# Kernel tuning notes

Hardware: AMD Instinct MI355X
Metric: run time of the kernel (lower is better)

The kernel has to match this reference:

```python
import jax, jax.numpy as jnp
import numpy as np

BS = 256
MAX_ARGS = 8
CTX_DIM = 128        # context_dim (local key/query dim)
NODE_DIM = 128       # node_dim (global query / embedding dim)
HIDDEN = 512
STATE_DIM = 512
TAC_DIM = 128
TOTAL_CTX = 131072   # total context nodes (~512 per batch element)
N_CLASS = 30000      # node_class_num
DEF_NUM = 20000      # len(global_context)
CTX_VAL_DIM = 256    # feature dim of context_emb.values
DIM = CTX_DIM + 1 + NODE_DIM  # 257


def setup_inputs() -> dict:
    key = jax.random.key(0)
    ks = jax.random.split(key, 12)
    ctx_ids = jnp.sort(jax.random.randint(ks[0], (TOTAL_CTX,), 0, BS)).astype(jnp.int32)
    ctx_vals = jax.random.normal(ks[1], (TOTAL_CTX, CTX_VAL_DIM), jnp.float32)
    state_emb = jax.random.normal(ks[2], (BS, STATE_DIM), jnp.float32)
    tactic_emb = jax.random.normal(ks[3], (BS, TAC_DIM), jnp.float32)
    arg_cnt = jax.random.randint(ks[4], (BS,), 0, MAX_ARGS + 1).astype(jnp.int32)
    global_context = jax.random.randint(ks[5], (DEF_NUM,), 0, N_CLASS).astype(jnp.int32)
    emb_table = jax.random.normal(ks[6], (N_CLASS, NODE_DIM), jnp.float32) * 0.05
    s1 = 1.0 / np.sqrt(CTX_VAL_DIM)
    W_key = jax.random.uniform(ks[7], (CTX_VAL_DIM, CTX_DIM), jnp.float32, -s1, s1)
    b_key = jnp.zeros((CTX_DIM,), jnp.float32)
    s2 = 1.0 / np.sqrt(STATE_DIM + TAC_DIM)
    W_st = jax.random.uniform(ks[8], (STATE_DIM + TAC_DIM, HIDDEN), jnp.float32, -s2, s2)
    b_st = jnp.zeros((HIDDEN,), jnp.float32)
    s3 = 1.0 / np.sqrt(HIDDEN)
    W_q = jax.random.uniform(ks[9], (HIDDEN, MAX_ARGS * DIM), jnp.float32, -s3, s3)
    b_q = jnp.zeros((MAX_ARGS * DIM,), jnp.float32)
    return dict(ctx_vals=ctx_vals, state_emb=state_emb, tactic_emb=tactic_emb,
                emb_table=emb_table, W_key=W_key, b_key=b_key, W_st=W_st, b_st=b_st,
                W_q=W_q, b_q=b_q, ctx_ids=ctx_ids, arg_cnt=arg_cnt,
                global_context=global_context)


def _build_indices(ctx_ids, arg_cnt, bs, max_args):
    """Host-side (numpy) reconstruction of the ragged index plumbing.
    Mirrors: sequence_mask/boolean_mask, unsorted_segment_sum, ragged.range,
    cumsum(exclusive) and the nested gathers of ArgumentLocalLogits."""
    ctx_ids = np.asarray(ctx_ids)
    arg_cnt = np.asarray(arg_cnt)
    # boolean_mask over [bs, max_args] sequence mask -> selected flat slots (row-major)
    mask = np.arange(max_args)[None, :] < arg_cnt[:, None]
    flat_sel = np.nonzero(mask.reshape(-1))[0]
    arguments_i = np.repeat(np.arange(bs), arg_cnt)          # batch id of each argument
    total_args = arguments_i.shape[0]
    ctx_lens = np.bincount(ctx_ids, minlength=bs)            # unsorted_segment_sum of ones
    ctx_starts = np.concatenate([[0], np.cumsum(ctx_lens)[:-1]])  # exclusive cumsum
    arg_ctx_lens = ctx_lens[arguments_i]
    arg_ctx_rows = np.repeat(np.arange(total_args), arg_ctx_lens)  # value_rowids of ragged.range
    pair_starts = np.concatenate([[0], np.cumsum(arg_ctx_lens)[:-1]])
    offs = np.arange(int(arg_ctx_lens.sum())) - np.repeat(pair_starts, arg_ctx_lens)
    arg_ctx_cols = ctx_starts[arguments_i][arg_ctx_rows] + offs
    return flat_sel, arg_ctx_rows, arg_ctx_cols, total_args


def reference(ctx_vals, state_emb, tactic_emb, emb_table, W_key, b_key,
              W_st, b_st, W_q, b_q, ctx_ids, arg_cnt, global_context):
    bs = state_emb.shape[0]
    flat_sel, rows, cols, total_args = _build_indices(ctx_ids, arg_cnt, bs, MAX_ARGS)
    gc = np.asarray(global_context)

    # state_tac_emb = relu(Dense(concat([state, tactic])))
    st = jax.nn.relu(jnp.concatenate([state_emb, tactic_emb], axis=1) @ W_st + b_st)
    # local_none_global: [bs, max_args, dim] -> boolean_mask -> [total_args, dim]
    lng = (st @ W_q + b_q).reshape(bs * MAX_ARGS, DIM)[flat_sel]
    local_queries = lng[:, :CTX_DIM]              # [total_args, CTX_DIM]
    none_logits = lng[:, CTX_DIM]                 # [total_args]
    global_queries = lng[:, CTX_DIM + 1:]         # [total_args, NODE_DIM]

    # local logits: gather-dot over (argument, context-node-of-its-batch) pairs
    keys = ctx_vals @ W_key + b_key               # act_key Dense: [total_ctx, CTX_DIM]
    local_flat = jnp.einsum('ij,ij->i', local_queries[rows], keys[cols])

    # global logits: unit-normalized embedding keys (normalize=True)
    gk = emb_table[gc]                            # [DEF_NUM, NODE_DIM]
    gk = gk / (1e-7 + jnp.sqrt(jnp.sum(gk * gk, axis=-1, keepdims=True)))
    global_flat = (global_queries @ gk.T).reshape(-1)  # row-major [total_args*DEF_NUM]

    indices = jnp.concatenate([
        jnp.asarray(rows, jnp.int32),
        jnp.arange(total_args, dtype=jnp.int32),
        jnp.asarray(np.repeat(np.arange(total_args), DEF_NUM), jnp.int32)])
    values = jnp.concatenate([local_flat, none_logits, global_flat])
    return indices, values
```

## Files before the change

### kernel.cpp

```cpp
#include <hip/hip_runtime.h>

#define BSZ 256
#define MAXA 8
#define CTXD 128
#define HID 512
#define STD 512
#define TACD 128
#define DEFN 20000
#define CVD 256
#define DIMQ 257
#define LNGW 2056

typedef __attribute__((ext_vector_type(8))) short bf16x8;
typedef __attribute__((ext_vector_type(4))) float f32x4;

#define O_TOT 0
#define O_NP  1
#define O_CS  16
#define O_AS  288
#define O_AB  560
#define O_SL  2608
#define O_PS  4656
#define F_GQB  8192
#define F_QB   139264
#define F_WST  141312
#define F_STB  305152
#define F_LNG  370688
#define F_WQT  897024
#define F_QK   897024
#define F_GKB  141312

__device__ __forceinline__ ushort f2bf(float f) {
    uint u = __float_as_uint(f);
    return (ushort)((u + 0x7FFFu + ((u >> 16) & 1u)) >> 16);
}

__global__ __launch_bounds__(256) void k_bounds(const int* __restrict__ ctx_ids, int n_ctx,
                                                int* __restrict__ W) {
    int i = blockIdx.x * 256 + threadIdx.x;
    if (i >= n_ctx) return;
    int cur = ctx_ids[i];
    int prev = (i == 0) ? -1 : ctx_ids[i - 1];
    for (int b = prev + 1; b <= cur; b++) W[O_CS + b] = i;
    if (i == n_ctx - 1) {
        for (int b = cur + 1; b <= BSZ; b++) W[O_CS + b] = n_ctx;
    }
}

__global__ __launch_bounds__(256) void k_scan(const int* __restrict__ arg_cnt, int* __restrict__ W) {
    __shared__ int s_start[BSZ + 1];
    __shared__ int s_len[BSZ];
    __shared__ int s_scan[BSZ];
    __shared__ int s_as[BSZ + 1];
    __shared__ int s_ab[2048];
    __shared__ int s_sl[2048];
    __shared__ int s_ps[BSZ];
    int tid = threadIdx.x;
    s_start[tid] = W[O_CS + tid];
    if (tid == 0) s_start[BSZ] = W[O_CS + BSZ];
    int c = arg_cnt[tid];
    s_scan[tid] = c;
    __syncthreads();
    s_len[tid] = s_start[tid + 1] - s_start[tid];
    for (int off = 1; off < BSZ; off <<= 1) {
        int v = s_scan[tid];
        int a = (tid >= off) ? s_scan[tid - off] : 0;
        __syncthreads();
        s_scan[tid] = v + a;
        __syncthreads();
    }
    int astart = s_scan[tid] - c;
    s_as[tid] = astart;
    if (tid == BSZ - 1) s_as[BSZ] = s_scan[tid];
    __syncthreads();
    int total = s_as[BSZ];
    for (int k = 0; k < c; k++) { s_ab[astart + k] = tid; s_sl[astart + k] = k; }
    __syncthreads();
    int base = tid * 8;
    int loc[8]; int run = 0;
    for (int j = 0; j < 8; j++) {
        int t = base + j;
        int l = (t < total) ? s_len[s_ab[t]] : 0;
        loc[j] = run; run += l;
    }
    s_ps[tid] = run;
    __syncthreads();
    for (int off = 1; off < BSZ; off <<= 1) {
        int v = s_ps[tid];
        int a = (tid >= off) ? s_ps[tid - off] : 0;
        __syncthreads();
        s_ps[tid] = v + a;
        __syncthreads();
    }
    int pbase = s_ps[tid] - run;
    int np = s_ps[BSZ - 1];
    W[O_AS + tid] = astart;
    if (tid == 0) { W[O_AS + BSZ] = total; W[O_TOT] = total; W[O_NP] = np; W[O_PS + 2048] = np; }
    for (int j = 0; j < 8; j++) {
        int t = base + j;
        W[O_PS + t] = pbase + loc[j];
        W[O_AB + t] = (t < total) ? s_ab[t] : 0;
        W[O_SL + t] = (t < total) ? s_sl[t] : 0;
    }
}

__global__ __launch_bounds__(256) void k_trans(const float* __restrict__ in, ushort* __restrict__ out,
                                               int R, int C) {
    __shared__ float t[32][33];
    int c0 = blockIdx.x * 32, r0 = blockIdx.y * 32;
    int lx = threadIdx.x & 31, ly = threadIdx.x >> 5;
    #pragma unroll
    for (int i = 0; i < 32; i += 8) {
        int r = r0 + ly + i, c = c0 + lx;
        t[ly + i][lx] = (r < R && c < C) ? in[(size_t)r * C + c] : 0.f;
    }
    __syncthreads();
    #pragma unroll
    for (int i = 0; i < 32; i += 8) {
        int oc = c0 + ly + i;
        int orr = r0 + lx;
        if (oc < C && orr < R) out[(size_t)oc * R + orr] = f2bf(t[lx][ly + i]);
    }
}

__device__ __forceinline__ bf16x8 cvt8(float4 a, float4 b) {
    bf16x8 r;
    r[0] = (short)f2bf(a.x); r[1] = (short)f2bf(a.y); r[2] = (short)f2bf(a.z); r[3] = (short)f2bf(a.w);
    r[4] = (short)f2bf(b.x); r[5] = (short)f2bf(b.y); r[6] = (short)f2bf(b.z); r[7] = (short)f2bf(b.w);
    return r;
}

__global__ __launch_bounds__(64) void k_fc1(const float* __restrict__ se, const float* __restrict__ te,
                                            const ushort* __restrict__ WstT, const float* __restrict__ bias,
                                            ushort* __restrict__ stb) {
    int bid = blockIdx.x;
    int m0 = (bid >> 4) * 16, n0 = (bid & 15) * 32;
    int lane = threadIdx.x;
    int lhi = lane >> 4, llo = lane & 15;
    f32x4 acc[2] = {};
    #pragma unroll
    for (int kk = 0; kk < 20; kk++) {
        int kb = kk * 32 + lhi * 8;
        const float* xr = (kb < 512) ? se + (size_t)(m0 + llo) * 512 + kb
                                     : te + (size_t)(m0 + llo) * 128 + (kb - 512);
        float4 x0 = *(const float4*)xr;
        float4 x1 = *(const float4*)(xr + 4);
        bf16x8 bfr = cvt8(x0, x1);
        #pragma unroll
        for (int nt = 0; nt < 2; nt++) {
            bf16x8 afr = *(const bf16x8*)(WstT + (size_t)(n0 + nt * 16 + llo) * 640 + kb);
            acc[nt] = __builtin_amdgcn_mfma_f32_16x16x32_bf16(afr, bfr, acc[nt], 0, 0, 0);
        }
    }
    #pragma unroll
    for (int nt = 0; nt < 2; nt++) {
        int n = n0 + nt * 16 + lhi * 4;
        float4 bb = *(const float4*)(bias + n);
        ushort4 o;
        o.x = f2bf(fmaxf(acc[nt][0] + bb.x, 0.f));
        o.y = f2bf(fmaxf(acc[nt][1] + bb.y, 0.f));
        o.z = f2bf(fmaxf(acc[nt][2] + bb.z, 0.f));
        o.w = f2bf(fmaxf(acc[nt][3] + bb.w, 0.f));
        *(ushort4*)(stb + (size_t)(m0 + llo) * 512 + n) = o;
    }
}

__global__ __launch_bounds__(64) void k_fc2(const ushort* __restrict__ stb, const ushort* __restrict__ WqT,
                                            const float* __restrict__ bias, float* __restrict__ LNG) {
    int n0 = blockIdx.x * 32, m0 = blockIdx.y * 16;
    int lane = threadIdx.x;
    int lhi = lane >> 4, llo = lane & 15;
    f32x4 acc[2] = {};
    #pragma unroll
    for (int kk = 0; kk < 16; kk++) {
        int kb = kk * 32 + lhi * 8;
        bf16x8 bfr = *(const bf16x8*)(stb + (size_t)(m0 + llo) * 512 + kb);
        #pragma unroll
        for (int nt = 0; nt < 2; nt++) {
            int n = n0 + nt * 16 + llo; if (n > 2055) n = 2055;
            bf16x8 afr = *(const bf16x8*)(WqT + (size_t)n * 512 + kb);
            acc[nt] = __builtin_amdgcn_mfma_f32_16x16x32_bf16(afr, bfr, acc[nt], 0, 0, 0);
        }
    }
    #pragma unroll
    for (int nt = 0; nt < 2; nt++) {
        int n = n0 + nt * 16 + lhi * 4;
        if (n < 2056) {
            float4 bb = *(const float4*)(bias + n);
            f32x4 v = {acc[nt][0] + bb.x, acc[nt][1] + bb.y, acc[nt][2] + bb.z, acc[nt][3] + bb.w};
            *(f32x4*)(LNG + (size_t)(m0 + llo) * 2056 + n) = v;
        }
    }
}

__global__ __launch_bounds__(256) void k_extract(const int* __restrict__ W, const float* __restrict__ LNG,
                                                 const float* __restrict__ Wkey, const float* __restrict__ bkey,
                                                 ushort* __restrict__ GQB, float* __restrict__ out, int L,
                                                 float* __restrict__ QK, float* __restrict__ QB) {
    int t = blockIdx.x;
    int total = W[O_TOT];
    int tid = threadIdx.x;
    if (t >= total) {
        if (tid >= 128) GQB[t * 128 + tid - 128] = 0;
        return;
    }
    int b = W[O_AB + t], slot = W[O_SL + t];
    const float* base = LNG + b * LNGW + slot * DIMQ;
    __shared__ float sl[CTXD];
    if (tid < 128) {
        sl[tid] = base[tid];
    } else {
        int d = tid - 128;
        GQB[t * 128 + d] = f2bf(base[129 + d]);
    }
    if (tid == 0) {
        int np = W[O_NP];
        out[np + t] = (float)t;
        out[L + np + t] = base[128];
    }
    __syncthreads();
    float acc = 0.f;
    const float* wr = Wkey + tid * 128;
    #pragma unroll
    for (int k = 0; k < 128; k += 4) {
        float4 w4 = *(const float4*)(wr + k);
        acc += w4.x * sl[k] + w4.y * sl[k + 1] + w4.z * sl[k + 2] + w4.w * sl[k + 3];
    }
    QK[t * 256 + tid] = acc;
    if (tid == 0) {
        float qb = 0.f;
        for (int k = 0; k < 128; k++) qb += bkey[k] * sl[k];
        QB[t] = qb;
    }
}

__global__ __launch_bounds__(256) void k_gk(const int* __restrict__ gctx, const float* __restrict__ emb,
                                            ushort* __restrict__ gkb) {
    int tid = threadIdx.x;
    int g = blockIdx.x * 8 + (tid >> 5);
    int row = gctx[g];
    int c = tid & 31;
    float4 e = *(const float4*)(emb + (size_t)row * 128 + c * 4);
    float ss = e.x * e.x + e.y * e.y + e.z * e.z + e.w * e.w;
    #pragma unroll
    for (int off = 1; off < 32; off <<= 1) ss += __shfl_xor(ss, off);
    float sc = 1.f / (1e-7f + sqrtf(ss));
    ushort4 o;
    o.x = f2bf(e.x * sc); o.y = f2bf(e.y * sc); o.z = f2bf(e.z * sc); o.w = f2bf(e.w * sc);
    *(ushort4*)(gkb + (size_t)g * 128 + c * 4) = o;
}

__global__ __launch_bounds__(256) void k_pairs(const int* __restrict__ W, const float* __restrict__ ctxv,
                                               const float* __restrict__ QK, const float* __restrict__ QB,
                                               float* __restrict__ out, int L) {
    int b = blockIdx.x >> 2, sub = blockIdx.x & 3;
    int as = W[O_AS + b];
    int cnt = W[O_AS + b + 1] - as;
    if (cnt == 0) return;
    int cs = W[O_CS + b];
    int len = W[O_CS + b + 1] - cs;
    int j0 = (len * sub) >> 2, j1 = (len * (sub + 1)) >> 2;
    __shared__ float sqk[MAXA][256];
    __shared__ float sqb[MAXA];
    __shared__ int sps[MAXA];
    int tid = threadIdx.x;
    for (int i = tid; i < cnt * 256; i += 256) sqk[i >> 8][i & 255] = QK[(as + (i >> 8)) * 256 + (i & 255)];
    if (tid < cnt) { sqb[tid] = QB[as + tid]; sps[tid] = W[O_PS + as + tid]; }
    __syncthreads();
    int wv = tid >> 6, lane = tid & 63;
    int g = lane >> 2, il = lane & 3;
    for (int jb = j0 + wv * 16; jb < j1; jb += 64) {
        int j = jb + g;
        bool ok = (j < j1);
        int row = cs + (ok ? j : j1 - 1);
        const float* xr = ctxv + (size_t)row * 256;
        float acc[MAXA] = {};
        #pragma unroll
        for (int c = 0; c < 16; c++) {
            float4 x4 = *(const float4*)(xr + c * 16 + il * 4);
            #pragma unroll
            for (int a = 0; a < MAXA; a++) {
                if (a < cnt) {
                    float4 q4 = *(const float4*)(&sqk[a][c * 16 + il * 4]);
                    acc[a] += x4.x * q4.x + x4.y * q4.y + x4.z * q4.z + x4.w * q4.w;
                }
            }
        }
        #pragma unroll
        for (int a = 0; a < MAXA; a++) {
            if (a < cnt) {
                float p = acc[a];
                p += __shfl_xor(p, 1);
                p += __shfl_xor(p, 2);
                if (il == 0 && ok) {
                    out[sps[a] + j] = (float)(as + a);
                    out[L + sps[a] + j] = p + sqb[a];
                }
            }
        }
    }
}

__global__ __launch_bounds__(256) void k_gglob(const int* __restrict__ W, const ushort* __restrict__ GQB,
                                               const ushort* __restrict__ GKB, float* __restrict__ out, int L) {
    __shared__ float tile[2][32][132];
    int total = W[O_TOT], np = W[O_NP];
    int t0 = blockIdx.y * 256;
    if (t0 >= total) return;
    float* outi = out + np + total;
    float* outv = out + L + np + total;
    int g0 = blockIdx.x * 128;
    int tid = threadIdx.x, wv = tid >> 6, lane = tid & 63;
    int lhi = lane >> 4, llo = lane & 15;
    int gw = wv * 32;
    bf16x8 afr[2][4];
    #pragma unroll
    for (int nt = 0; nt < 2; nt++) {
        int g = g0 + gw + nt * 16 + llo;
        const ushort* ap = GKB + (size_t)(g < DEFN ? g : DEFN - 1) * 128 + lhi * 8;
        #pragma unroll
        for (int kk = 0; kk < 4; kk++)
            afr[nt][kk] = *(const bf16x8*)(ap + kk * 32);
    }
    int nchunk = (total - t0 + 31) >> 5;
    if (nchunk > 8) nchunk = 8;
    bf16x8 bfr[2][4];
    #pragma unroll
    for (int ts = 0; ts < 2; ts++)
        #pragma unroll
        for (int kk = 0; kk < 4; kk++)
            bfr[ts][kk] = *(const bf16x8*)(GQB + (size_t)(t0 + ts * 16 + llo) * 128 + kk * 32 + lhi * 8);
    int half = lane >> 5, cc = (lane & 31) * 4;
    bool gok = (g0 + cc) < DEFN;
    for (int tc = 0; tc < nchunk; tc++) {
        int t1 = t0 + tc * 32;
        int buf = tc & 1;
        f32x4 acc[2][2] = {};
        #pragma unroll
        for (int nt = 0; nt < 2; nt++)
            #pragma unroll
            for (int kk = 0; kk < 4; kk++)
                #pragma unroll
                for (int ts = 0; ts < 2; ts++)
                    acc[ts][nt] = __builtin_amdgcn_mfma_f32_16x16x32_bf16(afr[nt][kk], bfr[ts][kk], acc[ts][nt], 0, 0, 0);
        if (tc + 1 < nchunk) {
            int t2 = t1 + 32;
            #pragma unroll
            for (int ts = 0; ts < 2; ts++)
                #pragma unroll
                for (int kk = 0; kk < 4; kk++)
                    bfr[ts][kk] = *(const bf16x8*)(GQB + (size_t)(t2 + ts * 16 + llo) * 128 + kk * 32 + lhi * 8);
        }
        #pragma unroll
        for (int nt = 0; nt < 2; nt++)
            #pragma unroll
            for (int ts = 0; ts < 2; ts++)
                *(f32x4*)&tile[buf][ts * 16 + llo][gw + nt * 16 + lhi * 4] = acc[ts][nt];
        __syncthreads();
        #pragma unroll
        for (int rp = 0; rp < 4; rp++) {
            int r = wv * 8 + rp * 2 + half;
            int t = t1 + r;
            if (t < total && gok) {
                size_t rb = (size_t)t * DEFN + g0 + cc;
                *(f32x4*)(outv + rb) = *(const f32x4*)&tile[buf][r][cc];
                float ft = (float)t;
                f32x4 fi = {ft, ft, ft, ft};
                *(f32x4*)(outi + rb) = fi;
            }
        }
    }
}

extern "C" void kernel_launch(void* const* d_in, const int* in_sizes, int n_in,
                              void* d_out, int out_size, void* d_ws, size_t ws_size,
                              hipStream_t stream) {
    const float* ctx_vals  = (const float*)d_in[0];
    const float* state_emb = (const float*)d_in[1];
    const float* tactic    = (const float*)d_in[2];
    const float* emb       = (const float*)d_in[3];
    const float* W_key     = (const float*)d_in[4];
    const float* b_key     = (const float*)d_in[5];
    const float* W_st      = (const float*)d_in[6];
    const float* b_st      = (const float*)d_in[7];
    const float* W_q       = (const float*)d_in[8];
    const float* b_q       = (const float*)d_in[9];
    const int* ctx_ids     = (const int*)d_in[10];
    const int* arg_cnt     = (const int*)d_in[11];
    const int* gctx        = (const int*)d_in[12];
    int n_ctx = in_sizes[10];
    int L = out_size / 2;
    int* W  = (int*)d_ws;
    float* F = (float*)d_ws;
    float* out = (float*)d_out;

    k_bounds<<<dim3((n_ctx + 255) / 256), dim3(256), 0, stream>>>(ctx_ids, n_ctx, W);
    k_scan<<<dim3(1), dim3(256), 0, stream>>>(arg_cnt, W);
    k_trans<<<dim3(16, 20), dim3(256), 0, stream>>>(W_st, (ushort*)(F + F_WST), 640, 512);
    k_trans<<<dim3(65, 16), dim3(256), 0, stream>>>(W_q, (ushort*)(F + F_WQT), 512, 2056);
    k_fc1<<<dim3(256), dim3(64), 0, stream>>>(state_emb, tactic, (ushort*)(F + F_WST), b_st,
                                              (ushort*)(F + F_STB));
    k_fc2<<<dim3(65, 16), dim3(64), 0, stream>>>((ushort*)(F + F_STB), (ushort*)(F + F_WQT), b_q,
                                                 F + F_LNG);
    k_extract<<<dim3(2048), dim3(256), 0, stream>>>(W, F + F_LNG, W_key, b_key,
                                                    (ushort*)(F + F_GQB), out, L, F + F_QK, F + F_QB);
    k_pairs<<<dim3(1024), dim3(256), 0, stream>>>(W, ctx_vals, F + F_QK, F + F_QB, out, L);
    k_gk<<<dim3(2500), dim3(256), 0, stream>>>(gctx, emb, (ushort*)(F + F_GKB));
    k_gglob<<<dim3(157, 8), dim3(256), 0, stream>>>(W, (ushort*)(F + F_GQB), (ushort*)(F + F_GKB), out, L);
}
```

Baseline: 152.9 us.

## Split global-logit index fill into separate kernel, store MFMA results directly

The global-logit kernel now writes MFMA accumulators straight to global memory instead of staging them through an LDS tile with a barrier. It uses finer row blocking (64 rows per block, 32 grid rows) for more parallelism. The index-value fill moves to a dedicated grid-stride kernel with contiguous vector stores. The two weight-transpose launches are merged into one 3D-grid kernel to cut launch count. Direct stores write 16-byte pieces scattered across rows, which may coalesce less well than the old LDS-staged row-contiguous writes.

```diff
diff --git a/kernel.cpp b/kernel.cpp
--- a/kernel.cpp
+++ b/kernel.cpp
@@ -104,8 +104,16 @@
     }
 }
 
-__global__ __launch_bounds__(256) void k_trans(const float* __restrict__ in, ushort* __restrict__ out,
-                                               int R, int C) {
+__global__ __launch_bounds__(256) void k_trans2(const float* __restrict__ Wst, ushort* __restrict__ oWst,
+                                                const float* __restrict__ Wq, ushort* __restrict__ oWq) {
+    const float* in; ushort* out; int R, C;
+    if (blockIdx.z == 0) {
+        in = Wst; out = oWst; R = 640; C = 512;
+        if (blockIdx.x >= 16 || blockIdx.y >= 20) return;
+    } else {
+        in = Wq; out = oWq; R = 512; C = 2056;
+        if (blockIdx.x >= 65 || blockIdx.y >= 16) return;
+    }
     __shared__ float t[32][33];
     int c0 = blockIdx.x * 32, r0 = blockIdx.y * 32;
     int lx = threadIdx.x & 31, ly = threadIdx.x >> 5;
@@ -303,11 +311,9 @@
 
 __global__ __launch_bounds__(256) void k_gglob(const int* __restrict__ W, const ushort* __restrict__ GQB,
                                                const ushort* __restrict__ GKB, float* __restrict__ out, int L) {
-    __shared__ float tile[2][32][132];
     int total = W[O_TOT], np = W[O_NP];
-    int t0 = blockIdx.y * 256;
+    int t0 = blockIdx.y * 64;
     if (t0 >= total) return;
-    float* outi = out + np + total;
     float* outv = out + L + np + total;
     int g0 = blockIdx.x * 128;
     int tid = threadIdx.x, wv = tid >> 6, lane = tid & 63;
@@ -323,18 +329,15 @@
             afr[nt][kk] = *(const bf16x8*)(ap + kk * 32);
     }
     int nchunk = (total - t0 + 31) >> 5;
-    if (nchunk > 8) nchunk = 8;
+    if (nchunk > 2) nchunk = 2;
     bf16x8 bfr[2][4];
     #pragma unroll
     for (int ts = 0; ts < 2; ts++)
         #pragma unroll
         for (int kk = 0; kk < 4; kk++)
             bfr[ts][kk] = *(const bf16x8*)(GQB + (size_t)(t0 + ts * 16 + llo) * 128 + kk * 32 + lhi * 8);
-    int half = lane >> 5, cc = (lane & 31) * 4;
-    bool gok = (g0 + cc) < DEFN;
     for (int tc = 0; tc < nchunk; tc++) {
         int t1 = t0 + tc * 32;
-        int buf = tc & 1;
         f32x4 acc[2][2] = {};
         #pragma unroll
         for (int nt = 0; nt < 2; nt++)
@@ -352,23 +355,31 @@
                     bfr[ts][kk] = *(const bf16x8*)(GQB + (size_t)(t2 + ts * 16 + llo) * 128 + kk * 32 + lhi * 8);
         }
         #pragma unroll
-        for (int nt = 0; nt < 2; nt++)
-            #pragma unroll
-            for (int ts = 0; ts < 2; ts++)
-                *(f32x4*)&tile[buf][ts * 16 + llo][gw + nt * 16 + lhi * 4] = acc[ts][nt];
-        __syncthreads();
-        #pragma unroll
-        for (int rp = 0; rp < 4; rp++) {
-            int r = wv * 8 + rp * 2 + half;
-            int t = t1 + r;
-            if (t < total && gok) {
-                size_t rb = (size_t)t * DEFN + g0 + cc;
-                *(f32x4*)(outv + rb) = *(const f32x4*)&tile[buf][r][cc];
-                float ft = (float)t;
-                f32x4 fi = {ft, ft, ft, ft};
-                *(f32x4*)(outi + rb) = fi;
+        for (int ts = 0; ts < 2; ts++) {
+            int t = t1 + ts * 16 + llo;
+            if (t < total) {
+                size_t rb = (size_t)t * DEFN;
+                #pragma unroll
+                for (int nt = 0; nt < 2; nt++) {
+                    int g = g0 + gw + nt * 16 + lhi * 4;
+                    if (g < DEFN) *(f32x4*)(outv + rb + g) = acc[ts][nt];
+                }
             }
         }
+    }
+}
+
+__global__ __launch_bounds__(256) void k_fillidx(const int* __restrict__ W, float* __restrict__ out, int L) {
+    int total = W[O_TOT], np = W[O_NP];
+    float* outi = out + np + total;
+    uint stride = gridDim.x * 256;
+    uint id0 = blockIdx.x * 256 + threadIdx.x;
+    uint n4 = (uint)total * (DEFN / 4);
+    for (uint i = id0; i < n4; i += stride) {
+        uint t = (i * 4u) / (uint)DEFN;
+        float ft = (float)t;
+        f32x4 v = {ft, ft, ft, ft};
+        *(f32x4*)(outi + (size_t)i * 4) = v;
     }
 }
 
@@ -396,8 +407,8 @@
 
     k_bounds<<<dim3((n_ctx + 255) / 256), dim3(256), 0, stream>>>(ctx_ids, n_ctx, W);
     k_scan<<<dim3(1), dim3(256), 0, stream>>>(arg_cnt, W);
-    k_trans<<<dim3(16, 20), dim3(256), 0, stream>>>(W_st, (ushort*)(F + F_WST), 640, 512);
-    k_trans<<<dim3(65, 16), dim3(256), 0, stream>>>(W_q, (ushort*)(F + F_WQT), 512, 2056);
+    k_trans2<<<dim3(65, 20, 2), dim3(256), 0, stream>>>(W_st, (ushort*)(F + F_WST),
+                                                        W_q, (ushort*)(F + F_WQT));
     k_fc1<<<dim3(256), dim3(64), 0, stream>>>(state_emb, tactic, (ushort*)(F + F_WST), b_st,
                                               (ushort*)(F + F_STB));
     k_fc2<<<dim3(65, 16), dim3(64), 0, stream>>>((ushort*)(F + F_STB), (ushort*)(F + F_WQT), b_q,
@@ -406,5 +417,6 @@
                                                     (ushort*)(F + F_GQB), out, L, F + F_QK, F + F_QB);
     k_pairs<<<dim3(1024), dim3(256), 0, stream>>>(W, ctx_vals, F + F_QK, F + F_QB, out, L);
     k_gk<<<dim3(2500), dim3(256), 0, stream>>>(gctx, emb, (ushort*)(F + F_GKB));
-    k_gglob<<<dim3(157, 8), dim3(256), 0, stream>>>(W, (ushort*)(F + F_GQB), (ushort*)(F + F_GKB), out, L);
-}
+    k_gglob<<<dim3(157, 32), dim3(256), 0, stream>>>(W, (ushort*)(F + F_GQB), (ushort*)(F + F_GKB), out, L);
+    k_fillidx<<<dim3(2048), dim3(256), 0, stream>>>(W, out, L);
+}
```

New measurement: 160.8 us. +5.1%, slower.
